# Kernel tuning notes

Hardware: AMD Instinct MI355X
Metric: run time of the kernel (lower is better)

## Reference

```python
import jax, jax.numpy as jnp
import numpy as np

LEAK = 0.95
NUM_STEPS = 10
THR = 1.0  # all layers get threshold = 1.0 in __init__

@jax.custom_vjp
def spike(x):
    # Surrogate_BP_Function.forward: heaviside(x > 0)
    return (x > 0).astype(x.dtype)

def _spike_fwd(x):
    return spike(x), x

def _spike_bwd(x, g):
    # backward: grad * 0.3 * relu(1 - |x|)
    return (g * 0.3 * jnp.maximum(1.0 - jnp.abs(x), 0.0),)

spike.defvjp(_spike_fwd, _spike_bwd)

def conv3x3(x, w):
    # stride 1, padding 1, no bias, NCHW / OIHW
    return jax.lax.conv_general_dilated(
        x, w, window_strides=(1, 1), padding=[(1, 1), (1, 1)],
        dimension_numbers=('NCHW', 'OIHW', 'NCHW'))

def avgpool2(x):
    b, c, h, w = x.shape
    return x.reshape(b, c, h // 2, 2, w // 2, 2).mean(axis=(3, 5))

def setup_inputs() -> dict:
    key = jax.random.key(0)
    ks = jax.random.split(key, 11)
    def w(k, shape, scale):
        return jax.random.normal(k, shape, dtype=jnp.float32) * scale
    inp = jax.random.normal(ks[0], (128, 3, 32, 32), dtype=jnp.float32)
    return {
        'inp': inp,
        'w1': w(ks[1], (64, 3, 3, 3), 0.35),
        'w2': w(ks[2], (64, 64, 3, 3), 0.1),
        'w3': w(ks[3], (128, 64, 3, 3), 0.1),
        'w4': w(ks[4], (128, 128, 3, 3), 0.08),
        'w5': w(ks[5], (256, 128, 3, 3), 0.08),
        'w6': w(ks[6], (256, 256, 3, 3), 0.06),
        'w7': w(ks[7], (256, 256, 3, 3), 0.06),
        'fc1_w': w(ks[8], (1024, 4096), 0.03),   # Linear(4*4*256, 1024)
        'fc2_w': w(ks[9], (10, 1024), 0.05),     # Linear(1024, 10)
    }

def reference(inp, w1, w2, w3, w4, w5, w6, w7, fc1_w, fc2_w):
    batch = inp.shape[0]
    conv_ws = [w2, w3, w4, w5, w6, w7]          # layers i = 1..6
    pool_after = [True, False, True, False, False, True]  # pool1 after i=1, pool2 after i=3, pool3 after i=6
    static = conv3x3(inp, w1)                   # static_input = conv1(inp)

    def step(carry, _):
        mem0, mem_fc1, mem_fc2 = carry
        # LIF update for conv1 (leaky accumulation of static input)
        mem0 = (1.0 - LEAK) * mem0 + LEAK * static
        thr = mem0 / THR - 1.0
        out_prev = spike(thr)
        mem0 = mem0 - jnp.where(thr > 0, THR, 0.0)  # soft reset
        # conv layers 2..7: membrane is OVERWRITTEN by the conv output each step
        for j, w in enumerate(conv_ws):
            m = conv3x3(out_prev, w)
            thr = m / THR - 1.0
            out_prev = spike(thr)
            if pool_after[j]:
                out_prev = avgpool2(out_prev)
        flat = out_prev.reshape(batch, -1)      # [B, 256*4*4]
        mem_fc1 = (1.0 - LEAK) * mem_fc1 + LEAK * (flat @ fc1_w.T)
        thr = mem_fc1 / THR - 1.0
        out = spike(thr)
        mem_fc1 = mem_fc1 - jnp.where(thr > 0, THR, 0.0)
        mem_fc2 = mem_fc2 + out @ fc2_w.T
        return (mem0, mem_fc1, mem_fc2), None

    init = (jnp.zeros_like(static),
            jnp.zeros((batch, 1024), dtype=inp.dtype),
            jnp.zeros((batch, fc2_w.shape[0]), dtype=inp.dtype))
    (mem0, mem_fc1, mem_fc2), _ = jax.lax.scan(step, init, None, length=NUM_STEPS)
    return mem_fc2 / NUM_STEPS
```

## Files before the change

kernel.cpp:

```cpp
#include <hip/hip_runtime.h>


typedef __attribute__((ext_vector_type(4))) int int32x4;

__device__ __forceinline__ float bf2f(ushort h) {
    union { unsigned u; float f; } v; v.u = ((unsigned)h) << 16;
    return v.f;
}
constexpr int ilog2(int x) { int r = 0; while (x > 1) { x >>= 1; ++r; } return r; }

__device__ __forceinline__ void gl_lds16(const void* g, void* l) {
    __builtin_amdgcn_global_load_lds(
        (const __attribute__((address_space(1))) unsigned int*)g,
        (__attribute__((address_space(3))) unsigned int*)l, 16, 0, 0);
}

#define SC21 4.76837158203125e-07
#define SC23 1.1920928955078125e-07

template <int IC, int OC>
__global__ void prep_convw_i8_k(const float* __restrict__ w, char* __restrict__ dst) {
    int idx = blockIdx.x * 256 + threadIdx.x;
    if (idx >= OC * IC * 9) return;
    int oc = idx / (IC * 9);
    int rem = idx % (IC * 9);
    int ic = rem / 9, q = rem % 9;
    int wq_ = (int)rintf(w[idx] * 2097152.0f);
    int a2 = ((wq_ + 128) & 255) - 128;
    int t2 = (wq_ - a2) >> 8;
    int a1 = ((t2 + 128) & 255) - 128;
    int a0 = (t2 - a1) >> 8;
    int sg = ic >> 6, kin = ic & 63, c = kin >> 4, bb = kin & 15;
    int oct = oc >> 6, ocl = oc & 63;
    constexpr int OCT = OC / 64;
    size_t base = ((size_t)(sg * 9 + q) * OCT + oct) * 12288;
    char digs[3] = {(char)a0, (char)a1, (char)a2};
#pragma unroll
    for (int s = 0; s < 3; ++s)
        dst[base + (size_t)(c * 192 + s * 64 + ocl) * 16 + bb] = digs[s];
}

__global__ void prep_fc1w_i8_k(const float* __restrict__ w, char* __restrict__ dst) {
    int idx = blockIdx.x * 256 + threadIdx.x;
    if (idx >= 1024 * 4096) return;
    int j = idx >> 12, k = idx & 4095;
    int c = k >> 4, hw = k & 15;
    int kp = hw * 256 + c;
    int wq_ = (int)rintf(w[idx] * 2097152.0f);
    int a2 = ((wq_ + 128) & 255) - 128;
    int t2 = (wq_ - a2) >> 8;
    int a1 = ((t2 + 128) & 255) - 128;
    int a0 = (t2 - a1) >> 8;
    int slab = kp >> 6, kin = kp & 63, cch = kin >> 4, bb = kin & 15;
    int oct = j >> 6, ocl = j & 63;
    size_t base = ((size_t)(slab * 16 + oct)) * 12288;
    char digs[3] = {(char)a0, (char)a1, (char)a2};
#pragma unroll
    for (int s = 0; s < 3; ++s)
        dst[base + (size_t)(cch * 192 + s * 64 + ocl) * 16 + bb] = digs[s];
}

template <int H, int C>
__global__ void halo0_k(char* __restrict__ buf) {
    constexpr int P = 4 * H + 4;
    constexpr int CPI = P * (C / 16);
    int idx = blockIdx.x * 256 + threadIdx.x;
    if (idx >= 1280 * CPI) return;
    int n = idx / CPI, r = idx % CPI;
    int p = r / (C / 16), c16 = r % (C / 16);
    int row, col;
    if (p < 2 * (H + 2)) { row = (p < H + 2) ? 0 : H + 1; col = p % (H + 2); }
    else { int qq = p - 2 * (H + 2); col = (qq < H) ? 0 : H + 1; row = 1 + (qq % H); }
    *(uint4*)&buf[(((size_t)n * (H + 2) + row) * (H + 2) + col) * C + c16 * 16] =
        (uint4){0u, 0u, 0u, 0u};
}

__global__ __launch_bounds__(256) void conv1lif_k(const float* __restrict__ inp,
                                                  const float* __restrict__ w1,
                                                  char* __restrict__ act1) {
    __shared__ float ws[27 * 64];
    for (int e = threadIdx.x; e < 1728; e += 256) {
        int oc = e / 27, j = e % 27;
        ws[j * 64 + oc] = w1[e];
    }
    __syncthreads();
    int t = blockIdx.x * 256 + threadIdx.x;
    int q = t & 3;
    int m = t >> 2;
    int n = m >> 10, h = (m >> 5) & 31, w = m & 31;
    float xv[27];
#pragma unroll
    for (int ic = 0; ic < 3; ++ic)
#pragma unroll
        for (int kh = 0; kh < 3; ++kh)
#pragma unroll
            for (int kw = 0; kw < 3; ++kw) {
                int r = h + kh - 1, c = w + kw - 1;
                xv[ic * 9 + kh * 3 + kw] =
                    (r >= 0 && r < 32 && c >= 0 && c < 32)
                        ? inp[(n * 3 + ic) * 1024 + r * 32 + c] : 0.0f;
            }
    float s[16], mem[16];
#pragma unroll
    for (int o = 0; o < 16; ++o) { s[o] = 0.f; mem[o] = 0.f; }
#pragma unroll
    for (int j = 0; j < 27; ++j) {
        float x = xv[j];
        const float* wr = &ws[j * 64 + q * 16];
#pragma unroll
        for (int o = 0; o < 16; ++o) s[o] += wr[o] * x;
    }
    const size_t dbase = (((size_t)h + 1) * 34 + (w + 1)) * 64 + q * 16;
    for (int st = 0; st < 10; ++st) {
        unsigned r[4];
#pragma unroll
        for (int g = 0; g < 4; ++g) {
            unsigned acc = 0;
#pragma unroll
            for (int e = 0; e < 4; ++e) {
                int o = g * 4 + e;
                mem[o] = 0.05f * mem[o] + 0.95f * s[o];
                unsigned b = (mem[o] > 1.f) ? 1u : 0u;
                mem[o] -= (float)b;
                acc |= b << (8 * e);
            }
            r[g] = acc;
        }
        size_t d = ((size_t)(st * 128 + n) * 34 * 34) * 64 + dbase;
        *(uint4*)&act1[d] = (uint4){r[0], r[1], r[2], r[3]};
    }
}

template <int H, int W, int IC, int OC, int NI, int MR, int EPI>
__global__ __launch_bounds__(256) void convi8_k(const char* __restrict__ act,
                                                const char* __restrict__ wq,
                                                char* __restrict__ outs,
                                                float scale) {
    constexpr int PW = W + 2, PHR = MR + 2;
    constexpr int MBLK = NI * MR * W;
    constexpr int NPIX = NI * PHR * PW;
    constexpr int ACH = NPIX * 4;
    constexpr int HR = (ACH + 255) / 256;
    constexpr int SLABS = IC / 64;
    constexpr int OCT = OC / 64;
    constexpr int U = SLABS * 9;
    constexpr int LHW = ilog2(H * W), LW2 = ilog2(W), LMW = ilog2(MR * W);
    static_assert(MBLK == 128, "tile mapping");

    __shared__ __align__(16) char sA[NPIX * 64];
    __shared__ __align__(16) char sB[3][12288];

    const int tid = threadIdx.x, lane = tid & 63;
    const int wid = tid >> 6, wm = wid >> 1, wn = wid & 1;
    const int b = blockIdx.x, oct = blockIdx.y;
    const int oc0 = oct * 64;
    const int m0 = b * MBLK;
    constexpr int TPI = (NI == 1) ? (H / MR) : 1;
    const int n0 = (NI == 1) ? (b / TPI) : (b * NI);
    const int h0 = (NI == 1) ? (b % TPI) * MR : 0;

    int asrc[HR]; bool apred[HR];
#pragma unroll
    for (int r = 0; r < HR; ++r) {
        int i = r * 256 + tid;
        apred[r] = (i < ACH);
        int ii = apred[r] ? i : 0;
        int c = ii / NPIX, pix = ii % NPIX;
        int pc = pix % PW, t2 = pix / PW;
        int hp = t2 % PHR, img = t2 / PHR;
        asrc[r] = (((n0 + img) * (H + 2) + h0 + hp) * PW + pc) * IC + c * 16;
    }
    int apix[4];
#pragma unroll
    for (int am = 0; am < 4; ++am) {
        int p = wm * 64 + am * 16 + (lane & 15);
        int img = p >> LMW;
        int pi = p & ((MR * W) - 1);
        int h = pi >> LW2;
        apix[am] = (img * PHR + h) * PW + (pi & (W - 1));
    }
    const int cA = lane >> 4;

    int32x4 acc[3][4][2];
#pragma unroll
    for (int s = 0; s < 3; ++s)
#pragma unroll
        for (int a = 0; a < 4; ++a)
#pragma unroll
            for (int bn = 0; bn < 2; ++bn) acc[s][a][bn] = (int32x4){0, 0, 0, 0};

    const size_t wqoct = (size_t)oct * 12288;

    auto stage_B = [&](int u_) {
        const char* wsrc = wq + (size_t)u_ * (OCT * 12288) + wqoct + tid * 16;
        char* d = sB[u_ % 3] + tid * 16;
        gl_lds16(wsrc, d);
        gl_lds16(wsrc + 4096, d + 4096);
        gl_lds16(wsrc + 8192, d + 8192);
    };
    auto stage_A = [&](int sl_) {
#pragma unroll
        for (int r = 0; r < HR; ++r)
            if (apred[r]) gl_lds16(act + asrc[r] + sl_ * 64, sA + (r * 256 + tid) * 16);
    };

    stage_A(0);
    stage_B(0);
    stage_B(1);

    for (int u = 0; u < U; ++u) {
        const int q = u - (u / 9) * 9;
        if (q == 0) asm volatile("s_waitcnt vmcnt(0)" ::: "memory");
        else        asm volatile("s_waitcnt vmcnt(3)" ::: "memory");
        __builtin_amdgcn_s_barrier();
        asm volatile("" ::: "memory");
        if (u + 2 < U) stage_B(u + 2);

        const int qr = q / 3, qc = q - qr * 3;
        int32x4 af[4];
#pragma unroll
        for (int am = 0; am < 4; ++am) {
            int pix = apix[am] + qr * PW + qc;
            af[am] = *(const int32x4*)&sA[(cA * NPIX + pix) * 16];
        }
        const char* bbase = sB[u % 3];
        __builtin_amdgcn_s_setprio(1);
#pragma unroll
        for (int s = 0; s < 3; ++s)
#pragma unroll
            for (int bn = 0; bn < 2; ++bn) {
                int R = s * 64 + wn * 32 + bn * 16 + (lane & 15);
                int32x4 bf = *(const int32x4*)&bbase[(cA * 192 + R) * 16];
#pragma unroll
                for (int am = 0; am < 4; ++am)
                    acc[s][am][bn] = __builtin_amdgcn_mfma_i32_16x16x64_i8(
                        af[am], bf, acc[s][am][bn], 0, 0, 0);
            }
        __builtin_amdgcn_s_setprio(0);

        if (q == 8 && u + 1 < U) {
            asm volatile("s_waitcnt lgkmcnt(0)" ::: "memory");
            __builtin_amdgcn_s_barrier();
            asm volatile("" ::: "memory");
            stage_A(u / 9 + 1);
        }
    }

#pragma unroll
    for (int am = 0; am < 4; ++am)
#pragma unroll
        for (int bn = 0; bn < 2; ++bn)
#pragma unroll
            for (int rr = 0; rr < 4; ++rr) {
                int rl = wm * 64 + am * 16 + (lane >> 4) * 4 + rr;
                int col = oc0 + wn * 32 + bn * 16 + (lane & 15);
                int m = m0 + rl;
                float v = (float)((65536.0 * (double)acc[0][am][bn][rr]
                                 + 256.0 * (double)acc[1][am][bn][rr]
                                 + (double)acc[2][am][bn][rr]) * (double)scale);
                char sp = (v > 1.0f) ? (char)1 : (char)0;
                if (EPI == 1) {
                    int n = m >> LHW, h = (m >> LW2) & (H - 1), w = m & (W - 1);
                    outs[((size_t)(n * (H + 2) + h + 1) * PW + (w + 1)) * OC + col] = sp;
                } else {
                    outs[(size_t)m * OC + col] = sp;
                }
            }
}

template <int C, int HI>
__global__ void pool_i8_k(const char* __restrict__ in, char* __restrict__ out) {
    constexpr int HO = HI / 2, C16 = C / 16;
    constexpr int TOT = 1280 * HO * HO * C16;
    int idx = blockIdx.x * 256 + threadIdx.x;
    if (idx >= TOT) return;
    int c16 = idx % C16;
    int t = idx / C16;
    int w = t % HO; t /= HO;
    int h = t % HO;
    int n = t / HO;
    const char* p = in + ((size_t)(n * HI + 2 * h) * HI + 2 * w) * C + c16 * 16;
    uint4 a0 = *(const uint4*)p;
    uint4 a1 = *(const uint4*)(p + C);
    uint4 a2 = *(const uint4*)(p + (size_t)HI * C);
    uint4 a3 = *(const uint4*)(p + (size_t)HI * C + C);
    uint4 r;
    r.x = a0.x + a1.x + a2.x + a3.x;
    r.y = a0.y + a1.y + a2.y + a3.y;
    r.z = a0.z + a1.z + a2.z + a3.z;
    r.w = a0.w + a1.w + a2.w + a3.w;
    *(uint4*)&out[((size_t)(n * (HO + 2) + h + 1) * (HO + 2) + (w + 1)) * C + c16 * 16] = r;
}

__global__ void pool3q_k(const char* __restrict__ in, char* __restrict__ out) {
    int idx = blockIdx.x * 256 + threadIdx.x;
    if (idx >= 327680) return;
    int c16 = idx & 15;
    int t = idx >> 4;
    int wo = t & 3, ho = (t >> 2) & 3, n = t >> 4;
    const char* p = in + ((size_t)(n * 8 + 2 * ho) * 8 + 2 * wo) * 256 + c16 * 16;
    uint4 a0 = *(const uint4*)p;
    uint4 a1 = *(const uint4*)(p + 256);
    uint4 a2 = *(const uint4*)(p + 2048);
    uint4 a3 = *(const uint4*)(p + 2048 + 256);
    uint4 r;
    r.x = a0.x + a1.x + a2.x + a3.x;
    r.y = a0.y + a1.y + a2.y + a3.y;
    r.z = a0.z + a1.z + a2.z + a3.z;
    r.w = a0.w + a1.w + a2.w + a3.w;
    *(uint4*)&out[((size_t)(n * 16 + ho * 4 + wo) * 16 + c16) * 16] = r;
}

__global__ __launch_bounds__(256) void fc1i8_k(const char* __restrict__ A,
                                               const char* __restrict__ wq,
                                               float* __restrict__ part) {
    __shared__ __align__(16) char sA[2][8192];
    __shared__ __align__(16) char sB[2][12288];
    const int tid = threadIdx.x, lane = tid & 63;
    const int wid = tid >> 6, wm = wid >> 1, wn = wid & 1;
    const int m0 = blockIdx.x * 128, oct = blockIdx.y, kt = blockIdx.z;

    int32x4 acc[3][4][2];
#pragma unroll
    for (int s = 0; s < 3; ++s)
#pragma unroll
        for (int a = 0; a < 4; ++a)
#pragma unroll
            for (int bn = 0; bn < 2; ++bn) acc[s][a][bn] = (int32x4){0, 0, 0, 0};

    auto stageA = [&](int sg, int bf_) {
#pragma unroll
        for (int r = 0; r < 2; ++r) {
            int i = r * 256 + tid;
            int c = i >> 7, pix = i & 127;
            gl_lds16(A + (size_t)(m0 + pix) * 4096 + sg * 64 + c * 16,
                     sA[bf_] + (size_t)i * 16);
        }
    };
    auto stageB = [&](int sg, int bf_) {
        const char* src = wq + ((size_t)(sg * 16 + oct)) * 12288 + tid * 16;
#pragma unroll
        for (int r = 0; r < 3; ++r)
            gl_lds16(src + r * 4096, sB[bf_] + (r * 256 + tid) * 16);
    };

    int buf = 0;
    stageA(kt * 32, 0);
    stageB(kt * 32, 0);
    __syncthreads();
    const int cA = lane >> 4;
    for (int sl = 0; sl < 32; ++sl) {
        int sg = kt * 32 + sl;
        if (sl < 31) { stageA(sg + 1, buf ^ 1); stageB(sg + 1, buf ^ 1); }
        int32x4 af[4];
#pragma unroll
        for (int am = 0; am < 4; ++am)
            af[am] = *(const int32x4*)&sA[buf][(cA * 128 + wm * 64 + am * 16 + (lane & 15)) * 16];
#pragma unroll
        for (int s = 0; s < 3; ++s)
#pragma unroll
            for (int bn = 0; bn < 2; ++bn) {
                int R = s * 64 + wn * 32 + bn * 16 + (lane & 15);
                int32x4 bf = *(const int32x4*)&sB[buf][(cA * 192 + R) * 16];
#pragma unroll
                for (int am = 0; am < 4; ++am)
                    acc[s][am][bn] = __builtin_amdgcn_mfma_i32_16x16x64_i8(
                        af[am], bf, acc[s][am][bn], 0, 0, 0);
            }
        if (sl < 31) { __syncthreads(); buf ^= 1; }
    }
#pragma unroll
    for (int am = 0; am < 4; ++am)
#pragma unroll
        for (int bn = 0; bn < 2; ++bn)
#pragma unroll
            for (int rr = 0; rr < 4; ++rr) {
                int row = m0 + wm * 64 + am * 16 + (lane >> 4) * 4 + rr;
                int col = oct * 64 + wn * 32 + bn * 16 + (lane & 15);
                float v = (float)((65536.0 * (double)acc[0][am][bn][rr]
                                 + 256.0 * (double)acc[1][am][bn][rr]
                                 + (double)acc[2][am][bn][rr]) * SC23);
                part[((size_t)kt * 1280 + row) * 1024 + col] = v;
            }
}

__global__ void fc1lif_k(const float* __restrict__ part, ushort* __restrict__ sbuf) {
    int idx = blockIdx.x * 256 + threadIdx.x;
    int n = idx >> 10, j = idx & 1023;
    float m = 0.f;
    for (int t = 0; t < 10; ++t) {
        size_t row = (size_t)(t * 128 + n) * 1024 + j;
        float y = part[row] + part[1310720 + row];
        m = 0.05f * m + 0.95f * y;
        float sp = (m > 1.f) ? 1.f : 0.f;
        m -= sp;
        sbuf[row] = sp > 0.f ? (ushort)0x3F80 : (ushort)0;
    }
}

__global__ __launch_bounds__(256) void fc2o_k(const ushort* __restrict__ S,
                                              const float* __restrict__ W2,
                                              float* __restrict__ out) {
    __shared__ float wsh[10 * 1024];
    __shared__ float red[10][256];
    int n = blockIdx.x, tid = threadIdx.x;
    for (int e = tid; e < 10240; e += 256) wsh[e] = W2[e];
    __syncthreads();
    float accv = 0.f;
    for (int t = 0; t < 10; ++t) {
        const ushort* sp = S + ((size_t)(t * 128 + n)) * 1024 + tid * 4;
        float s0 = bf2f(sp[0]), s1 = bf2f(sp[1]), s2 = bf2f(sp[2]), s3 = bf2f(sp[3]);
#pragma unroll
        for (int o = 0; o < 10; ++o) {
            const float* w = &wsh[o * 1024 + tid * 4];
            red[o][tid] = s0 * w[0] + s1 * w[1] + s2 * w[2] + s3 * w[3];
        }
        __syncthreads();
        for (int off = 128; off >= 1; off >>= 1) {
            if (tid < off) {
#pragma unroll
                for (int o = 0; o < 10; ++o) red[o][tid] += red[o][tid + off];
            }
            __syncthreads();
        }
        if (tid < 10) accv += red[tid][0];
        __syncthreads();
    }
    if (tid < 10) out[n * 10 + tid] = accv * 0.1f;
}

extern "C" void kernel_launch(void* const* d_in, const int* in_sizes, int n_in,
                              void* d_out, int out_size, void* d_ws, size_t ws_size,
                              hipStream_t stream) {
    const float* inp  = (const float*)d_in[0];
    const float* w1   = (const float*)d_in[1];
    const float* w2   = (const float*)d_in[2];
    const float* w3   = (const float*)d_in[3];
    const float* w4   = (const float*)d_in[4];
    const float* w5   = (const float*)d_in[5];
    const float* w6   = (const float*)d_in[6];
    const float* w7   = (const float*)d_in[7];
    const float* fc1w = (const float*)d_in[8];
    const float* fc2w = (const float*)d_in[9];
    float* out = (float*)d_out;

    char* base = (char*)d_ws;
    char* arenaA = base;
    char* arenaB = base + 94679040;
    size_t o = 94679040 + 83886080;
    auto alloc = [&](size_t bytes) { void* p = base + o; o += (bytes + 255) & ~(size_t)255; return p; };
    char*   wq2  = (char*)alloc(110592);
    char*   wq3  = (char*)alloc(221184);
    char*   wq4  = (char*)alloc(442368);
    char*   wq5  = (char*)alloc(884736);
    char*   wq6  = (char*)alloc(1769472);
    char*   wq7  = (char*)alloc(1769472);
    char*   wqf1 = (char*)alloc(12582912);
    ushort* sbuf = (ushort*)alloc(2621440);
    (void)ws_size;

    char*  act1  = arenaA;
    char*  c2out = arenaB;
    char*  act2  = arenaA;
    char*  c3out = arenaB;
    char*  c4out = arenaA;
    char*  act3  = arenaA + 41943040;
    char*  c5out = arenaB;
    char*  c6out = arenaB + 33554432;
    char*  c7out = arenaA;
    char*  afc1  = arenaA + 20971520;
    float* part  = (float*)(arenaA + 26214400);

    prep_convw_i8_k<64, 64>  <<<(36864 + 255) / 256, 256, 0, stream>>>(w2, wq2);
    prep_convw_i8_k<64, 128> <<<(73728 + 255) / 256, 256, 0, stream>>>(w3, wq3);
    prep_convw_i8_k<128, 128><<<(147456 + 255) / 256, 256, 0, stream>>>(w4, wq4);
    prep_convw_i8_k<128, 256><<<(294912 + 255) / 256, 256, 0, stream>>>(w5, wq5);
    prep_convw_i8_k<256, 256><<<(589824 + 255) / 256, 256, 0, stream>>>(w6, wq6);
    prep_convw_i8_k<256, 256><<<(589824 + 255) / 256, 256, 0, stream>>>(w7, wq7);
    prep_fc1w_i8_k<<<(4194304 + 255) / 256, 256, 0, stream>>>(fc1w, wqf1);

    halo0_k<32, 64><<<(1280 * 132 * 4 + 255) / 256, 256, 0, stream>>>(act1);
    conv1lif_k<<<2048, 256, 0, stream>>>(inp, w1, act1);

    convi8_k<32, 32, 64, 64, 1, 4, 0>
        <<<dim3(10240, 1), 256, 0, stream>>>(act1, wq2, c2out, (float)SC21);
    halo0_k<16, 64><<<(1280 * 68 * 4 + 255) / 256, 256, 0, stream>>>(act2);
    pool_i8_k<64, 32><<<(1280 * 256 * 4 + 255) / 256, 256, 0, stream>>>(c2out, act2);

    halo0_k<16, 128><<<(1280 * 68 * 8 + 255) / 256, 256, 0, stream>>>(c3out);
    convi8_k<16, 16, 64, 128, 1, 8, 1>
        <<<dim3(2560, 2), 256, 0, stream>>>(act2, wq3, c3out, (float)SC23);
    convi8_k<16, 16, 128, 128, 1, 8, 0>
        <<<dim3(2560, 2), 256, 0, stream>>>(c3out, wq4, c4out, (float)SC21);
    halo0_k<8, 128><<<(1280 * 36 * 8 + 255) / 256, 256, 0, stream>>>(act3);
    pool_i8_k<128, 16><<<(1280 * 64 * 8 + 255) / 256, 256, 0, stream>>>(c4out, act3);

    halo0_k<8, 256><<<(1280 * 36 * 16 + 255) / 256, 256, 0, stream>>>(c5out);
    convi8_k<8, 8, 128, 256, 2, 8, 1>
        <<<dim3(640, 4), 256, 0, stream>>>(act3, wq5, c5out, (float)SC23);
    halo0_k<8, 256><<<(1280 * 36 * 16 + 255) / 256, 256, 0, stream>>>(c6out);
    convi8_k<8, 8, 256, 256, 2, 8, 1>
        <<<dim3(640, 4), 256, 0, stream>>>(c5out, wq6, c6out, (float)SC21);
    convi8_k<8, 8, 256, 256, 2, 8, 0>
        <<<dim3(640, 4), 256, 0, stream>>>(c6out, wq7, c7out, (float)SC21);

    pool3q_k<<<(327680 + 255) / 256, 256, 0, stream>>>(c7out, afc1);

    fc1i8_k<<<dim3(10, 16, 2), 256, 0, stream>>>(afc1, wqf1, part);
    fc1lif_k<<<512, 256, 0, stream>>>(part, sbuf);
    fc2o_k<<<128, 256, 0, stream>>>(sbuf, fc2w, out);
}
```

Measured before the change: 887.4 us.

## Double-buffer LDS fragment reads in registers and unroll taps per slab

```diff
diff --git a/kernel.cpp b/kernel.cpp
--- a/kernel.cpp
+++ b/kernel.cpp
@@ -180,6 +180,7 @@
         apix[am] = (img * PHR + h) * PW + (pi & (W - 1));
     }
     const int cA = lane >> 4;
+    const int lan15 = lane & 15;
 
     int32x4 acc[3][4][2];
 #pragma unroll
@@ -189,11 +190,14 @@
 #pragma unroll
             for (int bn = 0; bn < 2; ++bn) acc[s][a][bn] = (int32x4){0, 0, 0, 0};
 
+    int32x4 afR[2][4];
+    int32x4 bfR[2][3][2];
+
     const size_t wqoct = (size_t)oct * 12288;
 
-    auto stage_B = [&](int u_) {
-        const char* wsrc = wq + (size_t)u_ * (OCT * 12288) + wqoct + tid * 16;
-        char* d = sB[u_ % 3] + tid * 16;
+    auto stage_B = [&](int unit, int bufc) {
+        const char* wsrc = wq + (size_t)unit * (OCT * 12288) + wqoct + tid * 16;
+        char* d = sB[bufc] + tid * 16;
         gl_lds16(wsrc, d);
         gl_lds16(wsrc + 4096, d + 4096);
         gl_lds16(wsrc + 8192, d + 8192);
@@ -203,46 +207,56 @@
         for (int r = 0; r < HR; ++r)
             if (apred[r]) gl_lds16(act + asrc[r] + sl_ * 64, sA + (r * 256 + tid) * 16);
     };
-
-    stage_A(0);
-    stage_B(0);
-    stage_B(1);
-
-    for (int u = 0; u < U; ++u) {
-        const int q = u - (u / 9) * 9;
-        if (q == 0) asm volatile("s_waitcnt vmcnt(0)" ::: "memory");
-        else        asm volatile("s_waitcnt vmcnt(3)" ::: "memory");
-        __builtin_amdgcn_s_barrier();
-        asm volatile("" ::: "memory");
-        if (u + 2 < U) stage_B(u + 2);
-
-        const int qr = q / 3, qc = q - qr * 3;
-        int32x4 af[4];
-#pragma unroll
-        for (int am = 0; am < 4; ++am) {
-            int pix = apix[am] + qr * PW + qc;
-            af[am] = *(const int32x4*)&sA[(cA * NPIX + pix) * 16];
-        }
-        const char* bbase = sB[u % 3];
+    auto prefetch = [&](int tapn, int setI, int bufc) {
+        const int qr = tapn / 3, qc = tapn - qr * 3;
+#pragma unroll
+        for (int am = 0; am < 4; ++am)
+            afR[setI][am] =
+                *(const int32x4*)&sA[(cA * NPIX + apix[am] + qr * PW + qc) * 16];
+#pragma unroll
+        for (int s = 0; s < 3; ++s)
+#pragma unroll
+            for (int bn = 0; bn < 2; ++bn)
+                bfR[setI][s][bn] = *(const int32x4*)
+                    &sB[bufc][(cA * 192 + s * 64 + wn * 32 + bn * 16 + lan15) * 16];
+    };
+    auto domfma = [&](int setI) {
         __builtin_amdgcn_s_setprio(1);
 #pragma unroll
         for (int s = 0; s < 3; ++s)
 #pragma unroll
-            for (int bn = 0; bn < 2; ++bn) {
-                int R = s * 64 + wn * 32 + bn * 16 + (lane & 15);
-                int32x4 bf = *(const int32x4*)&bbase[(cA * 192 + R) * 16];
+            for (int bn = 0; bn < 2; ++bn)
 #pragma unroll
                 for (int am = 0; am < 4; ++am)
                     acc[s][am][bn] = __builtin_amdgcn_mfma_i32_16x16x64_i8(
-                        af[am], bf, acc[s][am][bn], 0, 0, 0);
-            }
+                        afR[setI][am], bfR[setI][s][bn], acc[s][am][bn], 0, 0, 0);
         __builtin_amdgcn_s_setprio(0);
-
-        if (q == 8 && u + 1 < U) {
-            asm volatile("s_waitcnt lgkmcnt(0)" ::: "memory");
+    };
+
+    stage_A(0);
+    stage_B(0, 0);
+    stage_B(1, 1);
+    asm volatile("s_waitcnt vmcnt(0)" ::: "memory");
+    __builtin_amdgcn_s_barrier();
+    prefetch(0, 0, 0);
+
+    for (int sl = 0; sl < SLABS; ++sl) {
+        const int ub = sl * 9;
+#pragma unroll
+        for (int t = 0; t < 8; ++t) {
+            if (ub + t + 2 < U) stage_B(ub + t + 2, (t + 2) % 3);
+            prefetch(t + 1, (t + 1) & 1, (t + 1) % 3);
+            domfma(t & 1);
+            asm volatile("s_waitcnt vmcnt(0)" ::: "memory");
             __builtin_amdgcn_s_barrier();
-            asm volatile("" ::: "memory");
-            stage_A(u / 9 + 1);
+        }
+        if (ub + 10 < U) stage_B(ub + 10, 1);
+        if (sl + 1 < SLABS) stage_A(sl + 1);
+        domfma(0);
+        if (sl + 1 < SLABS) {
+            asm volatile("s_waitcnt vmcnt(0)" ::: "memory");
+            __builtin_amdgcn_s_barrier();
+            prefetch(0, 0, 0);
         }
     }
 
```

Result: slower. 1.143 ms (+28.8%).
